# Kernel tuning notes

Hardware: AMD Instinct MI355X
Metric: run time of the kernel (lower is better)

The kernel has to match this reference:

```python
import jax, jax.numpy as jnp
import numpy as np

EPS = 1e-12  # tf.nn.l2_normalize epsilon used by keras Dot(normalize=True)

def setup_inputs() -> dict:
    key = jax.random.key(0)
    k1, k2 = jax.random.split(key)
    a = jax.random.normal(k1, (16, 4096, 256), dtype=jnp.float32)
    b = jax.random.normal(k2, (16, 4096, 256), dtype=jnp.float32)
    return {"a": a, "b": b}

def _l2_normalize(x, axis=-1):
    # matches tf.nn.l2_normalize: x * rsqrt(max(sum(x^2), eps))
    sq = jnp.sum(x * x, axis=axis, keepdims=True)
    return x * jax.lax.rsqrt(jnp.maximum(sq, EPS))

def reference(a, b):
    # Original: full [B,N,N] cosine-similarity matrix then diag_part.
    # The diagonal equals the rowwise cosine similarity, computed directly.
    an = _l2_normalize(a, axis=2)  # [B, N, D]
    bn = _l2_normalize(b, axis=2)  # [B, N, D]
    return jnp.sum(an * bn, axis=2)  # [B, N]
```

## Files before the change

### kernel.cpp

```cpp
#include <hip/hip_runtime.h>


#define D 256
#define EPS 1e-12f

__global__ __launch_bounds__(256) void cosine_rows_kernel(
    const float* __restrict__ a,
    const float* __restrict__ b,
    float* __restrict__ out,
    int n_rows)
{
    const int lane = threadIdx.x & 63;
    const int wave = threadIdx.x >> 6;
    const int row  = blockIdx.x * 4 + wave;
    if (row >= n_rows) return;

    const float4* a4 = reinterpret_cast<const float4*>(a + (size_t)row * D);
    const float4* b4 = reinterpret_cast<const float4*>(b + (size_t)row * D);

    float4 av = a4[lane];
    float4 bv = b4[lane];

    float sa  = av.x * av.x + av.y * av.y + av.z * av.z + av.w * av.w;
    float sb  = bv.x * bv.x + bv.y * bv.y + bv.z * bv.z + bv.w * bv.w;
    float sab = av.x * bv.x + av.y * bv.y + av.z * bv.z + av.w * bv.w;

    #pragma unroll
    for (int off = 32; off > 0; off >>= 1) {
        sa  += __shfl_xor(sa,  off, 64);
        sb  += __shfl_xor(sb,  off, 64);
        sab += __shfl_xor(sab, off, 64);
    }

    if (lane == 0) {
        out[row] = sab * rsqrtf(fmaxf(sa, EPS)) * rsqrtf(fmaxf(sb, EPS));
    }
}

extern "C" void kernel_launch(void* const* d_in, const int* in_sizes, int n_in,
                              void* d_out, int out_size, void* d_ws, size_t ws_size,
                              hipStream_t stream)
{
    const float* a = (const float*)d_in[0];
    const float* b = (const float*)d_in[1];
    float* out = (float*)d_out;

    const int n_rows = out_size;
    const int rows_per_block = 4;
    const int grid = (n_rows + rows_per_block - 1) / rows_per_block;

    cosine_rows_kernel<<<grid, 256, 0, stream>>>(a, b, out, n_rows);
}
```

Before: 137.2 us.

## Assign one thread per row instead of one wavefront per row

Each thread now walks an entire 256-float row of a and b, accumulating the three sums serially with FMAs in register-batched chunks of eight float4 loads. This removes the cross-lane shuffle reduction and the idle lanes at the final store. In exchange, adjacent lanes read addresses 1 KB apart, so loads are no longer coalesced. The grid also shrinks to 256 blocks, which lowers the number of resident waves available to hide memory latency.

```diff
diff --git a/kernel.cpp b/kernel.cpp
--- a/kernel.cpp
+++ b/kernel.cpp
@@ -4,37 +4,36 @@
 #define D 256
 #define EPS 1e-12f
 
-__global__ __launch_bounds__(256) void cosine_rows_kernel(
+__global__ __launch_bounds__(256) void cosine_tpr_kernel(
     const float* __restrict__ a,
     const float* __restrict__ b,
     float* __restrict__ out,
     int n_rows)
 {
-    const int lane = threadIdx.x & 63;
-    const int wave = threadIdx.x >> 6;
-    const int row  = blockIdx.x * 4 + wave;
+    const int row = blockIdx.x * 256 + threadIdx.x;
     if (row >= n_rows) return;
 
     const float4* a4 = reinterpret_cast<const float4*>(a + (size_t)row * D);
     const float4* b4 = reinterpret_cast<const float4*>(b + (size_t)row * D);
 
-    float4 av = a4[lane];
-    float4 bv = b4[lane];
-
-    float sa  = av.x * av.x + av.y * av.y + av.z * av.z + av.w * av.w;
-    float sb  = bv.x * bv.x + bv.y * bv.y + bv.z * bv.z + bv.w * bv.w;
-    float sab = av.x * bv.x + av.y * bv.y + av.z * bv.z + av.w * bv.w;
+    float sa = 0.f, sb = 0.f, sab = 0.f;
 
     #pragma unroll
-    for (int off = 32; off > 0; off >>= 1) {
-        sa  += __shfl_xor(sa,  off, 64);
-        sb  += __shfl_xor(sb,  off, 64);
-        sab += __shfl_xor(sab, off, 64);
+    for (int c = 0; c < 8; ++c) {
+        float4 av[8], bv[8];
+        #pragma unroll
+        for (int j = 0; j < 8; ++j) av[j] = a4[c * 8 + j];
+        #pragma unroll
+        for (int j = 0; j < 8; ++j) bv[j] = b4[c * 8 + j];
+        #pragma unroll
+        for (int j = 0; j < 8; ++j) {
+            sa  = fmaf(av[j].x, av[j].x, fmaf(av[j].y, av[j].y, fmaf(av[j].z, av[j].z, fmaf(av[j].w, av[j].w, sa))));
+            sb  = fmaf(bv[j].x, bv[j].x, fmaf(bv[j].y, bv[j].y, fmaf(bv[j].z, bv[j].z, fmaf(bv[j].w, bv[j].w, sb))));
+            sab = fmaf(av[j].x, bv[j].x, fmaf(av[j].y, bv[j].y, fmaf(av[j].z, bv[j].z, fmaf(av[j].w, bv[j].w, sab))));
+        }
     }
 
-    if (lane == 0) {
-        out[row] = sab * rsqrtf(fmaxf(sa, EPS)) * rsqrtf(fmaxf(sb, EPS));
-    }
+    out[row] = sab * rsqrtf(fmaxf(sa, EPS)) * rsqrtf(fmaxf(sb, EPS));
 }
 
 extern "C" void kernel_launch(void* const* d_in, const int* in_sizes, int n_in,
@@ -46,8 +45,7 @@
     float* out = (float*)d_out;
 
     const int n_rows = out_size;
-    const int rows_per_block = 4;
-    const int grid = (n_rows + rows_per_block - 1) / rows_per_block;
+    const int grid = (n_rows + 255) / 256;
 
-    cosine_rows_kernel<<<grid, 256, 0, stream>>>(a, b, out, n_rows);
+    cosine_tpr_kernel<<<grid, 256, 0, stream>>>(a, b, out, n_rows);
 }
```

Result: slower. 156.3 us (+13.9%).

## Use persistent grid-stride waves with register double-buffered row prefetch

Applied to the files above, without the earlier changes.

Replaces the one-row-per-wave launch of 16384 blocks with a fixed grid of 2048 blocks whose waves stride over rows. Each wave loads the next row's a and b vectors into registers before reducing the current row, so memory latency overlaps with the shuffle reduction. The aim is to cut block launch overhead and keep more loads in flight per wave on this bandwidth-bound kernel. The cost is higher register use and fewer waves if the fixed grid does not fill the device.

```diff
diff --git a/kernel.cpp b/kernel.cpp
--- a/kernel.cpp
+++ b/kernel.cpp
@@ -4,36 +4,52 @@
 #define D 256
 #define EPS 1e-12f
 
-__global__ __launch_bounds__(256) void cosine_rows_kernel(
+__global__ __launch_bounds__(256, 8) void cosine_pers_kernel(
     const float* __restrict__ a,
     const float* __restrict__ b,
     float* __restrict__ out,
     int n_rows)
 {
-    const int lane = threadIdx.x & 63;
-    const int wave = threadIdx.x >> 6;
-    const int row  = blockIdx.x * 4 + wave;
+    const int lane   = threadIdx.x & 63;
+    const int gwave  = blockIdx.x * 4 + (threadIdx.x >> 6);
+    const int nwaves = gridDim.x * 4;
+
+    const float4* __restrict__ a4 = reinterpret_cast<const float4*>(a);
+    const float4* __restrict__ b4 = reinterpret_cast<const float4*>(b);
+
+    int row = gwave;
     if (row >= n_rows) return;
 
-    const float4* a4 = reinterpret_cast<const float4*>(a + (size_t)row * D);
-    const float4* b4 = reinterpret_cast<const float4*>(b + (size_t)row * D);
+    float4 av = a4[(size_t)row * 64 + lane];
+    float4 bv = b4[(size_t)row * 64 + lane];
 
-    float4 av = a4[lane];
-    float4 bv = b4[lane];
+    for (;;) {
+        const int  nrow = row + nwaves;
+        const bool more = (nrow < n_rows);
+        float4 av_n, bv_n;
+        if (more) {
+            av_n = a4[(size_t)nrow * 64 + lane];
+            bv_n = b4[(size_t)nrow * 64 + lane];
+        }
 
-    float sa  = av.x * av.x + av.y * av.y + av.z * av.z + av.w * av.w;
-    float sb  = bv.x * bv.x + bv.y * bv.y + bv.z * bv.z + bv.w * bv.w;
-    float sab = av.x * bv.x + av.y * bv.y + av.z * bv.z + av.w * bv.w;
+        float sa  = av.x*av.x + av.y*av.y + av.z*av.z + av.w*av.w;
+        float sb  = bv.x*bv.x + bv.y*bv.y + bv.z*bv.z + bv.w*bv.w;
+        float sab = av.x*bv.x + av.y*bv.y + av.z*bv.z + av.w*bv.w;
 
-    #pragma unroll
-    for (int off = 32; off > 0; off >>= 1) {
-        sa  += __shfl_xor(sa,  off, 64);
-        sb  += __shfl_xor(sb,  off, 64);
-        sab += __shfl_xor(sab, off, 64);
-    }
+        #pragma unroll
+        for (int off = 32; off > 0; off >>= 1) {
+            sa  += __shfl_xor(sa,  off, 64);
+            sb  += __shfl_xor(sb,  off, 64);
+            sab += __shfl_xor(sab, off, 64);
+        }
 
-    if (lane == 0) {
-        out[row] = sab * rsqrtf(fmaxf(sa, EPS)) * rsqrtf(fmaxf(sb, EPS));
+        if (lane == 0)
+            out[row] = sab * rsqrtf(fmaxf(sa, EPS)) * rsqrtf(fmaxf(sb, EPS));
+
+        if (!more) break;
+        row = nrow;
+        av = av_n;
+        bv = bv_n;
     }
 }
 
@@ -46,8 +62,9 @@
     float* out = (float*)d_out;
 
     const int n_rows = out_size;
-    const int rows_per_block = 4;
-    const int grid = (n_rows + rows_per_block - 1) / rows_per_block;
+    int grid = 2048;
+    const int max_grid = (n_rows + 3) / 4;
+    if (grid > max_grid) grid = max_grid;
 
-    cosine_rows_kernel<<<grid, 256, 0, stream>>>(a, b, out, n_rows);
+    cosine_pers_kernel<<<grid, 256, 0, stream>>>(a, b, out, n_rows);
 }
```

Result: slower. 144.5 us (+5.3%).
